# Kernel tuning notes

Hardware: AMD Instinct MI355X
Metric: run time of the kernel (lower is better)

The kernel has to match this reference:

```python
import jax, jax.numpy as jnp
import numpy as np

D_MODEL, D_K, D_V, N_HEADS = 1024, 64, 64, 16
BATCH, N_CTX = 2, 2048


def half_causal_allowed(n):
    # rows [0, n/2): attend to cols [0, n/2) only (dense block)
    # rows [n/2, n): standard causal (col <= row)
    i = jnp.arange(n)[:, None]
    j = jnp.arange(n)[None, :]
    top = (i < n // 2) & (j < n // 2)
    bot = (i >= n // 2) & (j <= i)
    return top | bot  # [n, n] bool


def setup_inputs() -> dict:
    key = jax.random.key(0)
    ks = jax.random.split(key, 8)
    s_in = 1.0 / np.sqrt(D_MODEL)
    s_out = 1.0 / np.sqrt(D_V * N_HEADS)
    return {
        "x": jax.random.normal(ks[0], (BATCH, N_CTX, D_MODEL), jnp.float32),
        # Linear weights stored [in, out] (transpose of torch layout)
        "Wq": jax.random.uniform(ks[1], (D_MODEL, D_K * N_HEADS), jnp.float32, -s_in, s_in),
        "bq": jax.random.uniform(ks[2], (D_K * N_HEADS,), jnp.float32, -s_in, s_in),
        "Wk": jax.random.uniform(ks[3], (D_MODEL, D_K * N_HEADS), jnp.float32, -s_in, s_in),
        "bk": jax.random.uniform(ks[4], (D_K * N_HEADS,), jnp.float32, -s_in, s_in),
        "Wv": jax.random.uniform(ks[5], (D_MODEL, D_V * N_HEADS), jnp.float32, -s_in, s_in),
        "bv": jax.random.uniform(ks[6], (D_V * N_HEADS,), jnp.float32, -s_in, s_in),
        "Wo": jax.random.uniform(ks[7], (D_V * N_HEADS, D_MODEL), jnp.float32, -s_out, s_out),
    }


def reference(x, Wq, bq, Wk, bk, Wv, bv, Wo):
    b, n, _ = x.shape
    h, dk, dv = N_HEADS, D_K, D_V
    # projections -> [b, h, n, d]
    q = (x @ Wq + bq).reshape(b, n, h, dk).transpose(0, 2, 1, 3)
    k = (x @ Wk + bk).reshape(b, n, h, dk).transpose(0, 2, 1, 3)
    v = (x @ Wv + bv).reshape(b, n, h, dv).transpose(0, 2, 1, 3)
    scores = jnp.einsum("bhqd,bhkd->bhqk", q / jnp.sqrt(jnp.float32(dk)), k)
    allowed = half_causal_allowed(n)  # [n, n]
    scores = jnp.where(allowed, scores, -jnp.inf)
    attn = jax.nn.softmax(scores, axis=-1)  # dropout p=0 -> identity
    out = jnp.einsum("bhqk,bhkd->bhqd", attn, v)
    out = out.transpose(0, 2, 1, 3).reshape(b, n, h * dv)
    return out @ Wo  # final Linear has no bias
```

## Files before the change

kernel.cpp:

```cpp
#include <hip/hip_runtime.h>
#include <hip/hip_bf16.h>

#define NH 16
#define DH 64
#define DM 1024
#define NC 2048
#define MROWS 4096
#define KVT 64

#define SCALE_Q 0.180336880f

typedef __attribute__((ext_vector_type(8))) short short8;
typedef __attribute__((ext_vector_type(4))) float f32x4;
typedef __attribute__((ext_vector_type(16))) float f32x16;
typedef __attribute__((ext_vector_type(4))) unsigned int uint4e;

__device__ __forceinline__ unsigned pkbf16(float a, float b) {
    unsigned r;
    asm("v_cvt_pk_bf16_f32 %0, %1, %2" : "=v"(r) : "v"(a), "v"(b));
    return r;
}
__device__ __forceinline__ unsigned short f2bf(float x) {
    return (unsigned short)(pkbf16(x, x) & 0xffffu);
}
__device__ __forceinline__ float exp2v(float x) {
    float r;
    asm("v_exp_f32 %0, %1" : "=v"(r) : "v"(x));
    return r;
}
__device__ __forceinline__ f32x16 fzero16() {
    f32x16 r;
    #pragma unroll
    for (int i = 0; i < 16; ++i) r[i] = 0.f;
    return r;
}
__device__ __forceinline__ short8 mk8(unsigned w0, unsigned w1, unsigned w2, unsigned w3) {
    uint4e u = {w0, w1, w2, w3};
    return __builtin_bit_cast(short8, u);
}
__device__ __forceinline__ void gload16(const unsigned short* g, unsigned short* l) {
    __builtin_amdgcn_global_load_lds(
        (const __attribute__((address_space(1))) void*)g,
        (__attribute__((address_space(3))) void*)l, 16, 0, 0);
}

__global__ __launch_bounds__(256) void cvt_x(const float* __restrict__ in,
                                             unsigned short* __restrict__ out, int n8)
{
    int i = blockIdx.x * 256 + threadIdx.x;
    if (i >= n8) return;
    const float4 a = ((const float4*)in)[i * 2];
    const float4 b = ((const float4*)in)[i * 2 + 1];
    uint4e u = {pkbf16(a.x, a.y), pkbf16(a.z, a.w), pkbf16(b.x, b.y), pkbf16(b.z, b.w)};
    ((uint4e*)out)[i] = u;
}

__global__ __launch_bounds__(256) void cvt_w4(const float* __restrict__ W0,
                                              const float* __restrict__ W1,
                                              const float* __restrict__ W2,
                                              const float* __restrict__ W3,
                                              unsigned short* __restrict__ Wt4)
{
    __shared__ unsigned short T[64][72];
    const int z = blockIdx.z;
    const float* W = (z == 0) ? W0 : (z == 1) ? W1 : (z == 2) ? W2 : W3;
    unsigned short* Wt = Wt4 + (size_t)z * DM * DM;
    const int t = threadIdx.x;
    const int r = t >> 2, s = t & 3;
    const int bi = blockIdx.y;
    const int bj = blockIdx.x;
    const float* src = W + (size_t)(bi * 64 + r) * DM + bj * 64 + s * 16;
    float4 f0 = ((const float4*)src)[0];
    float4 f1 = ((const float4*)src)[1];
    float4 f2 = ((const float4*)src)[2];
    float4 f3 = ((const float4*)src)[3];
    uint2 u;
    u.x = pkbf16(f0.x, f0.y); u.y = pkbf16(f0.z, f0.w); *(uint2*)&T[r][s * 16]      = u;
    u.x = pkbf16(f1.x, f1.y); u.y = pkbf16(f1.z, f1.w); *(uint2*)&T[r][s * 16 + 4]  = u;
    u.x = pkbf16(f2.x, f2.y); u.y = pkbf16(f2.z, f2.w); *(uint2*)&T[r][s * 16 + 8]  = u;
    u.x = pkbf16(f3.x, f3.y); u.y = pkbf16(f3.z, f3.w); *(uint2*)&T[r][s * 16 + 12] = u;
    __syncthreads();
    unsigned short vals[16];
    #pragma unroll
    for (int j = 0; j < 16; ++j) vals[j] = T[s * 16 + j][r];
    unsigned short* dst = Wt + (size_t)(bj * 64 + r) * DM + bi * 64 + s * 16;
    *(short8*)(dst)     = *(short8*)&vals[0];
    *(short8*)(dst + 8) = *(short8*)&vals[8];
}

__global__ __launch_bounds__(256) void gemm_qkv(const unsigned short* __restrict__ A,
                                                const unsigned short* __restrict__ Bt,
                                                const float* __restrict__ bq,
                                                const float* __restrict__ bk,
                                                const float* __restrict__ bv,
                                                unsigned short* __restrict__ Out)
{
    __shared__ unsigned short As[128 * 32];
    __shared__ unsigned short Bs[128 * 32];
    const int t  = threadIdx.x;
    const int w  = t >> 6, l = t & 63;
    const int wr = w >> 1, wc = w & 1;
    const int m0 = blockIdx.y << 7;
    const int n0 = blockIdx.x << 7;

    f32x4 acc[4][4] = {};
    const int nkt = DM >> 5;
    for (int kt = 0; kt < nkt; ++kt) {
        #pragma unroll
        for (int j = 0; j < 2; ++j) {
            const int c0 = j * 256 + w * 64;
            const int cc = c0 + l;
            const int row = cc >> 2, qq = cc & 3;
            gload16(A  + (size_t)(m0 + row) * DM + kt * 32 + qq * 8, &As[c0 * 8]);
            gload16(Bt + (size_t)(n0 + row) * DM + kt * 32 + qq * 8, &Bs[c0 * 8]);
        }
        __syncthreads();
        short8 af[4], bf_[4];
        #pragma unroll
        for (int mi = 0; mi < 4; ++mi)
            af[mi] = *(short8*)&As[(wr * 64 + mi * 16 + (l & 15)) * 32 + (l >> 4) * 8];
        #pragma unroll
        for (int ni = 0; ni < 4; ++ni)
            bf_[ni] = *(short8*)&Bs[(wc * 64 + ni * 16 + (l & 15)) * 32 + (l >> 4) * 8];
        #pragma unroll
        for (int mi = 0; mi < 4; ++mi)
            #pragma unroll
            for (int ni = 0; ni < 4; ++ni)
                acc[mi][ni] = __builtin_amdgcn_mfma_f32_16x16x32_bf16(
                                  af[mi], bf_[ni], acc[mi][ni], 0, 0, 0);
        __syncthreads();
    }

    const int seg = n0 >> 10;
    const float* bias = (seg == 0) ? bq : (seg == 1) ? bk : bv;
    const float scale = (seg == 0) ? SCALE_Q : 1.0f;
    const int ncol0 = (n0 & 1023) + wc * 64;
    float bvv[4];
    #pragma unroll
    for (int ni = 0; ni < 4; ++ni)
        bvv[ni] = bias[ncol0 + ni * 16 + (l & 15)];

    if (seg == 2) {
        unsigned short* vt = Out + 2 * (size_t)MROWS * DM;
        #pragma unroll
        for (int mi = 0; mi < 4; ++mi)
            #pragma unroll
            for (int ni = 0; ni < 4; ++ni) {
                const int gcol = ncol0 + ni * 16 + (l & 15);
                const int h_ = gcol >> 6, d_ = gcol & 63;
                #pragma unroll
                for (int r = 0; r < 4; ++r) {
                    const int grow = m0 + wr * 64 + mi * 16 + (l >> 4) * 4 + r;
                    const int b_ = grow >> 11, n_ = grow & 2047;
                    vt[(((size_t)b_ * 16 + h_) * 64 + d_) * NC + n_] =
                        f2bf(acc[mi][ni][r] + bvv[ni]);
                }
            }
    } else {
        unsigned short* C = Out + (size_t)seg * MROWS * DM;
        #pragma unroll
        for (int mi = 0; mi < 4; ++mi)
            #pragma unroll
            for (int ni = 0; ni < 4; ++ni) {
                const int gcol = ncol0 + ni * 16 + (l & 15);
                #pragma unroll
                for (int r = 0; r < 4; ++r) {
                    const int grow = m0 + wr * 64 + mi * 16 + (l >> 4) * 4 + r;
                    C[(size_t)grow * DM + gcol] = f2bf((acc[mi][ni][r] + bvv[ni]) * scale);
                }
            }
    }
}

__global__ __launch_bounds__(256) void gemm_wo(const unsigned short* __restrict__ A,
                                               const unsigned short* __restrict__ Bt,
                                               float* __restrict__ C)
{
    __shared__ unsigned short As[64 * 32];
    __shared__ unsigned short Bs[128 * 32];
    const int t = threadIdx.x, w = t >> 6, l = t & 63;
    const int wr = w >> 1, wc = w & 1;
    const int m0 = blockIdx.y << 6;
    const int n0 = blockIdx.x << 7;

    f32x4 acc[2][4] = {};
    const int nkt = DM >> 5;
    for (int kt = 0; kt < nkt; ++kt) {
        {
            const int c0 = w * 64;
            const int cc = c0 + l;
            const int row = cc >> 2, qq = cc & 3;
            gload16(A + (size_t)(m0 + row) * DM + kt * 32 + qq * 8, &As[c0 * 8]);
        }
        #pragma unroll
        for (int j = 0; j < 2; ++j) {
            const int c0 = j * 256 + w * 64;
            const int cc = c0 + l;
            const int row = cc >> 2, qq = cc & 3;
            gload16(Bt + (size_t)(n0 + row) * DM + kt * 32 + qq * 8, &Bs[c0 * 8]);
        }
        __syncthreads();
        short8 af[2], bf_[4];
        #pragma unroll
        for (int mi = 0; mi < 2; ++mi)
            af[mi] = *(short8*)&As[(wr * 32 + mi * 16 + (l & 15)) * 32 + (l >> 4) * 8];
        #pragma unroll
        for (int ni = 0; ni < 4; ++ni)
            bf_[ni] = *(short8*)&Bs[(wc * 64 + ni * 16 + (l & 15)) * 32 + (l >> 4) * 8];
        #pragma unroll
        for (int mi = 0; mi < 2; ++mi)
            #pragma unroll
            for (int ni = 0; ni < 4; ++ni)
                acc[mi][ni] = __builtin_amdgcn_mfma_f32_16x16x32_bf16(
                                  af[mi], bf_[ni], acc[mi][ni], 0, 0, 0);
        __syncthreads();
    }
    #pragma unroll
    for (int mi = 0; mi < 2; ++mi)
        #pragma unroll
        for (int ni = 0; ni < 4; ++ni) {
            const int gcol = n0 + wc * 64 + ni * 16 + (l & 15);
            #pragma unroll
            for (int r = 0; r < 4; ++r) {
                const int grow = m0 + wr * 32 + mi * 16 + (l >> 4) * 4 + r;
                C[(size_t)grow * DM + gcol] = acc[mi][ni][r];
            }
        }
}

__global__ __launch_bounds__(128, 2) void attn_nosm(const unsigned short* __restrict__ Qg,
                                                    const unsigned short* __restrict__ Kg,
                                                    const unsigned short* __restrict__ Vtg,
                                                    unsigned short* __restrict__ Og)
{
    __shared__ unsigned short KS[2][4096];
    __shared__ unsigned short VS[2][4096];
    const int t   = threadIdx.x;
    const int w   = t >> 6;
    const int l   = t & 63;
    const int l31 = l & 31;
    const int hi  = l >> 5;

    const int f   = blockIdx.x;
    const int xcd = f & 7;
    const int pos = f >> 3;
    const int bh  = xcd * 4 + (pos >> 5);
    int qt = pos & 31;
    if ((pos >> 5) & 1) qt = 31 - qt;
    const int b = bh >> 4;
    const int h = bh & 15;

    const int qb = qt << 6;
    const int wq = qb + w * 32;
    const size_t rb0 = (size_t)b * NC;
    const int hd = h * DH;

    const unsigned short* qp = Qg + (rb0 + wq + l31) * DM + hd + hi * 8;
    short8 fq[4];
    #pragma unroll
    for (int c = 0; c < 4; ++c)
        fq[c] = *(const short8*)(qp + c * 16);

    f32x16 o0 = fzero16(), o1 = fzero16();
    f32x16 lacc = fzero16();
    const bool bottom = (qb >= NC / 2);
    const int nkv = bottom ? (qt + 1) : 16;

    const unsigned short* Vbase = Vtg + (size_t)bh * 64 * NC;

    auto stage = [&](int it, int buf) {
        const int kb = it * KVT;
        #pragma unroll
        for (int j = 0; j < 4; ++j) {
            const int jj  = w * 4 + j;
            const int p   = jj * 64 + l;
            const int row = p >> 3;
            const int slot = (p & 7) ^ (row & 7);
            gload16(Kg + (size_t)(rb0 + kb + row) * DM + hd + slot * 8,
                    &KS[buf][jj * 512]);
            gload16(Vbase + (size_t)row * NC + kb + slot * 8,
                    &VS[buf][jj * 512]);
        }
    };

    stage(0, 0);
    if (nkv > 1) stage(1, 1);

    for (int it = 0; it < nkv; ++it) {
        const int kb = it * KVT;
        const int cur = it & 1;
        if (it + 1 < nkv) {
            asm volatile("s_waitcnt vmcnt(8)" ::: "memory");
        } else {
            asm volatile("s_waitcnt vmcnt(0)" ::: "memory");
        }
        __builtin_amdgcn_s_barrier();

        short8 kf[2][4], vf[2][4];
        #pragma unroll
        for (int half = 0; half < 2; ++half) {
            const int row = half * 32 + l31;
            const int rx  = row & 7;
            #pragma unroll
            for (int c = 0; c < 4; ++c) {
                const int slot = (c * 2 + hi) ^ rx;
                kf[half][c] = *(const short8*)(&KS[cur][row * 64 + slot * 8]);
                vf[half][c] = *(const short8*)(&VS[cur][row * 64 + slot * 8]);
            }
        }
        asm volatile("s_waitcnt lgkmcnt(0)" ::: "memory");
        __builtin_amdgcn_sched_barrier(0);
        __builtin_amdgcn_s_barrier();

        if (it + 2 < nkv) stage(it + 2, cur);

        const bool active = bottom ? (kb <= wq + 31) : true;
        if (active) {
            f32x16 s0 = fzero16(), s1 = fzero16();
            __builtin_amdgcn_s_setprio(1);
            #pragma unroll
            for (int c = 0; c < 4; ++c) {
                s0 = __builtin_amdgcn_mfma_f32_32x32x16_bf16(kf[0][c], fq[c], s0, 0, 0, 0);
                s1 = __builtin_amdgcn_mfma_f32_32x32x16_bf16(kf[1][c], fq[c], s1, 0, 0, 0);
            }
            __builtin_amdgcn_s_setprio(0);
            if (bottom && (kb + KVT - 1 > wq)) {
                const int qg = wq + l31;
                #pragma unroll
                for (int r = 0; r < 16; ++r) {
                    const int kk = (r & 3) + 8 * (r >> 2) + 4 * hi;
                    if (kb + kk > qg)      s0[r] = -1e30f;
                    if (kb + 32 + kk > qg) s1[r] = -1e30f;
                }
            }
            #pragma unroll
            for (int r = 0; r < 16; ++r) s0[r] = exp2v(s0[r]);
            #pragma unroll
            for (int r = 0; r < 16; ++r) s1[r] = exp2v(s1[r]);
            #pragma unroll
            for (int r = 0; r < 16; ++r) lacc[r] += s0[r] + s1[r];
            __builtin_amdgcn_s_setprio(1);
            #pragma unroll
            for (int kc = 0; kc < 4; ++kc) {
                const f32x16 src = (kc < 2) ? s0 : s1;
                const int rbase = (kc & 1) * 8;
                unsigned A01 = pkbf16(src[rbase + 0], src[rbase + 1]);
                unsigned A23 = pkbf16(src[rbase + 2], src[rbase + 3]);
                unsigned A45 = pkbf16(src[rbase + 4], src[rbase + 5]);
                unsigned A67 = pkbf16(src[rbase + 6], src[rbase + 7]);
                unsigned s01 = (unsigned)__shfl_xor((int)A01, 32);
                unsigned s23 = (unsigned)__shfl_xor((int)A23, 32);
                unsigned s45 = (unsigned)__shfl_xor((int)A45, 32);
                unsigned s67 = (unsigned)__shfl_xor((int)A67, 32);
                short8 fp = hi ? mk8(s45, s67, A45, A67)
                               : mk8(A01, A23, s01, s23);
                o0 = __builtin_amdgcn_mfma_f32_32x32x16_bf16(vf[0][kc], fp, o0, 0, 0, 0);
                o1 = __builtin_amdgcn_mfma_f32_32x32x16_bf16(vf[1][kc], fp, o1, 0, 0, 0);
            }
            __builtin_amdgcn_s_setprio(0);
        }
    }
    __syncthreads();

    float lr[8];
    #pragma unroll
    for (int r = 0; r < 8; ++r) lr[r] = lacc[r] + lacc[r + 8];
    #pragma unroll
    for (int st = 4; st > 0; st >>= 1)
        #pragma unroll
        for (int r = 0; r < 4; ++r)
            if (r < st) lr[r] += lr[r + st];
    const float lrun = lr[0] + __shfl_xor(lr[0], 32);
    const float inv = 1.f / lrun;

    unsigned short* obuf = (unsigned short*)&KS[0][0];
    {
        unsigned short* reg = obuf + (size_t)(w * 32 + l31) * 72;
        #pragma unroll
        for (int r = 0; r < 16; ++r) {
            const int dd = (r & 3) + 8 * (r >> 2) + 4 * hi;
            reg[dd]      = f2bf(o0[r] * inv);
            reg[dd + 32] = f2bf(o1[r] * inv);
        }
    }
    __syncthreads();
    {
        const int row = t >> 1, seg = t & 1;
        const unsigned short* src = obuf + (size_t)row * 72 + seg * 32;
        unsigned short* dst = Og + (rb0 + qb + row) * DM + hd + seg * 32;
        #pragma unroll
        for (int i = 0; i < 4; ++i)
            *(short8*)(dst + i * 8) = *(const short8*)(src + i * 8);
    }
}

extern "C" void kernel_launch(void* const* d_in, const int* in_sizes, int n_in,
                              void* d_out, int out_size, void* d_ws, size_t ws_size,
                              hipStream_t stream)
{
    const float* x  = (const float*)d_in[0];
    const float* Wq = (const float*)d_in[1];
    const float* bq = (const float*)d_in[2];
    const float* Wk = (const float*)d_in[3];
    const float* bk = (const float*)d_in[4];
    const float* Wv = (const float*)d_in[5];
    const float* bv = (const float*)d_in[6];
    const float* Wo = (const float*)d_in[7];
    float* out = (float*)d_out;

    char* ws = (char*)d_ws;
    const size_t szA = (size_t)MROWS * DM * 2;
    const size_t szW = (size_t)DM * DM * 2;
    unsigned short* xb  = (unsigned short*)(ws);
    unsigned short* wqT = (unsigned short*)(ws + szA);
    unsigned short* woT = (unsigned short*)(ws + szA + 3 * szW);
    unsigned short* qb_ = (unsigned short*)(ws + szA + 4 * szW);
    unsigned short* kb_ = (unsigned short*)(ws + 2 * szA + 4 * szW);
    unsigned short* vt_ = (unsigned short*)(ws + 3 * szA + 4 * szW);
    unsigned short* ab_ = (unsigned short*)(ws + 4 * szA + 4 * szW);

    cvt_x<<<dim3(MROWS * DM / 8 / 256), 256, 0, stream>>>(x, xb, MROWS * DM / 8);
    cvt_w4<<<dim3(16, 16, 4), 256, 0, stream>>>(Wq, Wk, Wv, Wo, wqT);

    gemm_qkv<<<dim3(24, 32), 256, 0, stream>>>(xb, wqT, bq, bk, bv, qb_);
    attn_nosm<<<dim3(1024), 128, 0, stream>>>(qb_, kb_, vt_, ab_);
    gemm_wo<<<dim3(8, 64), 256, 0, stream>>>(ab_, woT, out);
}
```

Measured before the change: 114.7 us.

## Split attention KV loop across two waves per 32-row query tile; fuse prep kernels

The attention kernel now gives each block a 32-row query tile and has its two waves process alternating KV tiles independently, each with its own LDS buffer and no block barriers in the loop. The partial outputs and row sums are combined through LDS at the end. This doubles the grid, cuts the per-block causal tail, and removes inter-wave synchronisation. The price is that each wave loads full K/V tiles (no shared staging), there is only single-buffer prefetch per wave, and an extra reduction step. Separately, the x and weight bf16 conversion kernels are merged into a single launch.

```diff
diff --git a/kernel.cpp b/kernel.cpp
--- a/kernel.cpp
+++ b/kernel.cpp
@@ -44,31 +44,35 @@
         (__attribute__((address_space(3))) void*)l, 16, 0, 0);
 }
 
-__global__ __launch_bounds__(256) void cvt_x(const float* __restrict__ in,
-                                             unsigned short* __restrict__ out, int n8)
-{
-    int i = blockIdx.x * 256 + threadIdx.x;
-    if (i >= n8) return;
-    const float4 a = ((const float4*)in)[i * 2];
-    const float4 b = ((const float4*)in)[i * 2 + 1];
-    uint4e u = {pkbf16(a.x, a.y), pkbf16(a.z, a.w), pkbf16(b.x, b.y), pkbf16(b.z, b.w)};
-    ((uint4e*)out)[i] = u;
-}
-
-__global__ __launch_bounds__(256) void cvt_w4(const float* __restrict__ W0,
-                                              const float* __restrict__ W1,
-                                              const float* __restrict__ W2,
-                                              const float* __restrict__ W3,
-                                              unsigned short* __restrict__ Wt4)
+__global__ __launch_bounds__(256) void prep(const float* __restrict__ x,
+                                            const float* __restrict__ W0,
+                                            const float* __restrict__ W1,
+                                            const float* __restrict__ W2,
+                                            const float* __restrict__ W3,
+                                            unsigned short* __restrict__ xb,
+                                            unsigned short* __restrict__ Wt4)
 {
     __shared__ unsigned short T[64][72];
-    const int z = blockIdx.z;
+    const int bid = blockIdx.x;
+    const int t = threadIdx.x;
+    if (bid < 1024) {
+        #pragma unroll
+        for (int g = 0; g < 2; ++g) {
+            const int i = bid * 512 + g * 256 + t;
+            const float4 a = ((const float4*)x)[i * 2];
+            const float4 b = ((const float4*)x)[i * 2 + 1];
+            uint4e u = {pkbf16(a.x, a.y), pkbf16(a.z, a.w),
+                        pkbf16(b.x, b.y), pkbf16(b.z, b.w)};
+            ((uint4e*)xb)[i] = u;
+        }
+        return;
+    }
+    const int z = (bid - 1024) >> 8;
+    const int tile = (bid - 1024) & 255;
+    const int bi = tile >> 4, bj = tile & 15;
     const float* W = (z == 0) ? W0 : (z == 1) ? W1 : (z == 2) ? W2 : W3;
     unsigned short* Wt = Wt4 + (size_t)z * DM * DM;
-    const int t = threadIdx.x;
     const int r = t >> 2, s = t & 3;
-    const int bi = blockIdx.y;
-    const int bj = blockIdx.x;
     const float* src = W + (size_t)(bi * 64 + r) * DM + bj * 64 + s * 16;
     float4 f0 = ((const float4*)src)[0];
     float4 f1 = ((const float4*)src)[1];
@@ -228,10 +232,10 @@
         }
 }
 
-__global__ __launch_bounds__(128, 2) void attn_nosm(const unsigned short* __restrict__ Qg,
-                                                    const unsigned short* __restrict__ Kg,
-                                                    const unsigned short* __restrict__ Vtg,
-                                                    unsigned short* __restrict__ Og)
+__global__ __launch_bounds__(128) void attn_split(const unsigned short* __restrict__ Qg,
+                                                  const unsigned short* __restrict__ Kg,
+                                                  const unsigned short* __restrict__ Vtg,
+                                                  unsigned short* __restrict__ Og)
 {
     __shared__ unsigned short KS[2][4096];
     __shared__ unsigned short VS[2][4096];
@@ -244,18 +248,17 @@
     const int f   = blockIdx.x;
     const int xcd = f & 7;
     const int pos = f >> 3;
-    const int bh  = xcd * 4 + (pos >> 5);
-    int qt = pos & 31;
-    if ((pos >> 5) & 1) qt = 31 - qt;
+    const int bh  = xcd * 4 + (pos >> 6);
+    int qc = pos & 63;
+    if ((pos >> 6) & 1) qc = 63 - qc;
     const int b = bh >> 4;
     const int h = bh & 15;
 
-    const int qb = qt << 6;
-    const int wq = qb + w * 32;
+    const int qb = qc << 5;
     const size_t rb0 = (size_t)b * NC;
     const int hd = h * DH;
 
-    const unsigned short* qp = Qg + (rb0 + wq + l31) * DM + hd + hi * 8;
+    const unsigned short* qp = Qg + (rb0 + qb + l31) * DM + hd + hi * 8;
     short8 fq[4];
     #pragma unroll
     for (int c = 0; c < 4; ++c)
@@ -263,38 +266,31 @@
 
     f32x16 o0 = fzero16(), o1 = fzero16();
     f32x16 lacc = fzero16();
-    const bool bottom = (qb >= NC / 2);
-    const int nkv = bottom ? (qt + 1) : 16;
+    const int nkv = (qc < 32) ? 16 : ((qc >> 1) + 1);
+    const int niter = (nkv - w + 1) >> 1;
 
     const unsigned short* Vbase = Vtg + (size_t)bh * 64 * NC;
 
-    auto stage = [&](int it, int buf) {
+    auto stage = [&](int it) {
         const int kb = it * KVT;
         #pragma unroll
-        for (int j = 0; j < 4; ++j) {
-            const int jj  = w * 4 + j;
-            const int p   = jj * 64 + l;
-            const int row = p >> 3;
+        for (int j = 0; j < 8; ++j) {
+            const int p    = j * 64 + l;
+            const int row  = p >> 3;
             const int slot = (p & 7) ^ (row & 7);
             gload16(Kg + (size_t)(rb0 + kb + row) * DM + hd + slot * 8,
-                    &KS[buf][jj * 512]);
+                    &KS[w][j * 512]);
             gload16(Vbase + (size_t)row * NC + kb + slot * 8,
-                    &VS[buf][jj * 512]);
+                    &VS[w][j * 512]);
         }
     };
 
-    stage(0, 0);
-    if (nkv > 1) stage(1, 1);
-
-    for (int it = 0; it < nkv; ++it) {
+    stage(w);
+
+    for (int i = 0; i < niter; ++i) {
+        const int it = w + 2 * i;
         const int kb = it * KVT;
-        const int cur = it & 1;
-        if (it + 1 < nkv) {
-            asm volatile("s_waitcnt vmcnt(8)" ::: "memory");
-        } else {
-            asm volatile("s_waitcnt vmcnt(0)" ::: "memory");
-        }
-        __builtin_amdgcn_s_barrier();
+        asm volatile("s_waitcnt vmcnt(0)" ::: "memory");
 
         short8 kf[2][4], vf[2][4];
         #pragma unroll
@@ -304,63 +300,57 @@
             #pragma unroll
             for (int c = 0; c < 4; ++c) {
                 const int slot = (c * 2 + hi) ^ rx;
-                kf[half][c] = *(const short8*)(&KS[cur][row * 64 + slot * 8]);
-                vf[half][c] = *(const short8*)(&VS[cur][row * 64 + slot * 8]);
+                kf[half][c] = *(const short8*)(&KS[w][row * 64 + slot * 8]);
+                vf[half][c] = *(const short8*)(&VS[w][row * 64 + slot * 8]);
             }
         }
         asm volatile("s_waitcnt lgkmcnt(0)" ::: "memory");
         __builtin_amdgcn_sched_barrier(0);
-        __builtin_amdgcn_s_barrier();
-
-        if (it + 2 < nkv) stage(it + 2, cur);
-
-        const bool active = bottom ? (kb <= wq + 31) : true;
-        if (active) {
-            f32x16 s0 = fzero16(), s1 = fzero16();
-            __builtin_amdgcn_s_setprio(1);
-            #pragma unroll
-            for (int c = 0; c < 4; ++c) {
-                s0 = __builtin_amdgcn_mfma_f32_32x32x16_bf16(kf[0][c], fq[c], s0, 0, 0, 0);
-                s1 = __builtin_amdgcn_mfma_f32_32x32x16_bf16(kf[1][c], fq[c], s1, 0, 0, 0);
+        if (i + 1 < niter) stage(w + 2 * (i + 1));
+
+        f32x16 s0 = fzero16(), s1 = fzero16();
+        __builtin_amdgcn_s_setprio(1);
+        #pragma unroll
+        for (int c = 0; c < 4; ++c) {
+            s0 = __builtin_amdgcn_mfma_f32_32x32x16_bf16(kf[0][c], fq[c], s0, 0, 0, 0);
+            s1 = __builtin_amdgcn_mfma_f32_32x32x16_bf16(kf[1][c], fq[c], s1, 0, 0, 0);
+        }
+        __builtin_amdgcn_s_setprio(0);
+        if (qc >= 32 && it == nkv - 1) {
+            const int qg = qb + l31;
+            #pragma unroll
+            for (int r = 0; r < 16; ++r) {
+                const int kk = (r & 3) + 8 * (r >> 2) + 4 * hi;
+                if (kb + kk > qg)      s0[r] = -1e30f;
+                if (kb + 32 + kk > qg) s1[r] = -1e30f;
             }
-            __builtin_amdgcn_s_setprio(0);
-            if (bottom && (kb + KVT - 1 > wq)) {
-                const int qg = wq + l31;
-                #pragma unroll
-                for (int r = 0; r < 16; ++r) {
-                    const int kk = (r & 3) + 8 * (r >> 2) + 4 * hi;
-                    if (kb + kk > qg)      s0[r] = -1e30f;
-                    if (kb + 32 + kk > qg) s1[r] = -1e30f;
-                }
-            }
-            #pragma unroll
-            for (int r = 0; r < 16; ++r) s0[r] = exp2v(s0[r]);
-            #pragma unroll
-            for (int r = 0; r < 16; ++r) s1[r] = exp2v(s1[r]);
-            #pragma unroll
-            for (int r = 0; r < 16; ++r) lacc[r] += s0[r] + s1[r];
-            __builtin_amdgcn_s_setprio(1);
-            #pragma unroll
-            for (int kc = 0; kc < 4; ++kc) {
-                const f32x16 src = (kc < 2) ? s0 : s1;
-                const int rbase = (kc & 1) * 8;
-                unsigned A01 = pkbf16(src[rbase + 0], src[rbase + 1]);
-                unsigned A23 = pkbf16(src[rbase + 2], src[rbase + 3]);
-                unsigned A45 = pkbf16(src[rbase + 4], src[rbase + 5]);
-                unsigned A67 = pkbf16(src[rbase + 6], src[rbase + 7]);
-                unsigned s01 = (unsigned)__shfl_xor((int)A01, 32);
-                unsigned s23 = (unsigned)__shfl_xor((int)A23, 32);
-                unsigned s45 = (unsigned)__shfl_xor((int)A45, 32);
-                unsigned s67 = (unsigned)__shfl_xor((int)A67, 32);
-                short8 fp = hi ? mk8(s45, s67, A45, A67)
-                               : mk8(A01, A23, s01, s23);
-                o0 = __builtin_amdgcn_mfma_f32_32x32x16_bf16(vf[0][kc], fp, o0, 0, 0, 0);
-                o1 = __builtin_amdgcn_mfma_f32_32x32x16_bf16(vf[1][kc], fp, o1, 0, 0, 0);
-            }
-            __builtin_amdgcn_s_setprio(0);
-        }
-    }
-    __syncthreads();
+        }
+        #pragma unroll
+        for (int r = 0; r < 16; ++r) s0[r] = exp2v(s0[r]);
+        #pragma unroll
+        for (int r = 0; r < 16; ++r) s1[r] = exp2v(s1[r]);
+        #pragma unroll
+        for (int r = 0; r < 16; ++r) lacc[r] += s0[r] + s1[r];
+        __builtin_amdgcn_s_setprio(1);
+        #pragma unroll
+        for (int kc = 0; kc < 4; ++kc) {
+            const f32x16 src = (kc < 2) ? s0 : s1;
+            const int rbase = (kc & 1) * 8;
+            unsigned A01 = pkbf16(src[rbase + 0], src[rbase + 1]);
+            unsigned A23 = pkbf16(src[rbase + 2], src[rbase + 3]);
+            unsigned A45 = pkbf16(src[rbase + 4], src[rbase + 5]);
+            unsigned A67 = pkbf16(src[rbase + 6], src[rbase + 7]);
+            unsigned s01 = (unsigned)__shfl_xor((int)A01, 32);
+            unsigned s23 = (unsigned)__shfl_xor((int)A23, 32);
+            unsigned s45 = (unsigned)__shfl_xor((int)A45, 32);
+            unsigned s67 = (unsigned)__shfl_xor((int)A67, 32);
+            short8 fp = hi ? mk8(s45, s67, A45, A67)
+                           : mk8(A01, A23, s01, s23);
+            o0 = __builtin_amdgcn_mfma_f32_32x32x16_bf16(vf[0][kc], fp, o0, 0, 0, 0);
+            o1 = __builtin_amdgcn_mfma_f32_32x32x16_bf16(vf[1][kc], fp, o1, 0, 0, 0);
+        }
+        __builtin_amdgcn_s_setprio(0);
+    }
 
     float lr[8];
     #pragma unroll
@@ -370,22 +360,38 @@
         #pragma unroll
         for (int r = 0; r < 4; ++r)
             if (r < st) lr[r] += lr[r + st];
-    const float lrun = lr[0] + __shfl_xor(lr[0], 32);
-    const float inv = 1.f / lrun;
-
-    unsigned short* obuf = (unsigned short*)&KS[0][0];
+    const float lpart = lr[0] + __shfl_xor(lr[0], 32);
+
     {
-        unsigned short* reg = obuf + (size_t)(w * 32 + l31) * 72;
+        float* po = (float*)&KS[w][0];
+        #pragma unroll
+        for (int r = 0; r < 16; ++r) {
+            po[l * 32 + r]      = o0[r];
+            po[l * 32 + 16 + r] = o1[r];
+        }
+        ((float*)&VS[w][0])[l] = lpart;
+    }
+    __syncthreads();
+
+    if (w == 0) {
+        const float* po1 = (const float*)&KS[1][0];
+        float oc0[16], oc1[16];
+        #pragma unroll
+        for (int r = 0; r < 16; ++r) {
+            oc0[r] = o0[r] + po1[l * 32 + r];
+            oc1[r] = o1[r] + po1[l * 32 + 16 + r];
+        }
+        const float lt = lpart + ((const float*)&VS[1][0])[l];
+        const float inv = 1.f / lt;
+        unsigned short* obuf = &VS[0][0];
+        unsigned short* reg = obuf + (size_t)l31 * 72;
         #pragma unroll
         for (int r = 0; r < 16; ++r) {
             const int dd = (r & 3) + 8 * (r >> 2) + 4 * hi;
-            reg[dd]      = f2bf(o0[r] * inv);
-            reg[dd + 32] = f2bf(o1[r] * inv);
-        }
-    }
-    __syncthreads();
-    {
-        const int row = t >> 1, seg = t & 1;
+            reg[dd]      = f2bf(oc0[r] * inv);
+            reg[dd + 32] = f2bf(oc1[r] * inv);
+        }
+        const int row = l >> 1, seg = l & 1;
         const unsigned short* src = obuf + (size_t)row * 72 + seg * 32;
         unsigned short* dst = Og + (rb0 + qb + row) * DM + hd + seg * 32;
         #pragma unroll
@@ -419,10 +425,8 @@
     unsigned short* vt_ = (unsigned short*)(ws + 3 * szA + 4 * szW);
     unsigned short* ab_ = (unsigned short*)(ws + 4 * szA + 4 * szW);
 
-    cvt_x<<<dim3(MROWS * DM / 8 / 256), 256, 0, stream>>>(x, xb, MROWS * DM / 8);
-    cvt_w4<<<dim3(16, 16, 4), 256, 0, stream>>>(Wq, Wk, Wv, Wo, wqT);
-
+    prep<<<dim3(2048), 256, 0, stream>>>(x, Wq, Wk, Wv, Wo, xb, wqT);
     gemm_qkv<<<dim3(24, 32), 256, 0, stream>>>(xb, wqT, bq, bk, bv, qb_);
-    attn_nosm<<<dim3(1024), 128, 0, stream>>>(qb_, kb_, vt_, ab_);
+    attn_split<<<dim3(2048), 128, 0, stream>>>(qb_, kb_, vt_, ab_);
     gemm_wo<<<dim3(8, 64), 256, 0, stream>>>(ab_, woT, out);
 }
```

Result: slower. 118.9 us (+3.7%).

## Double GEMM K-tile to 64 with XOR-swizzled LDS and merge prep kernels

Applied to the files above, without the earlier changes.

Both GEMMs now stage 64-wide K tiles instead of 32, which halves the loop iterations and the barriers per tile. The LDS layout uses an XOR swizzle on 16-byte slots to avoid bank conflicts on the fragment reads. The x conversion and the weight-transpose kernels are merged into one launch to save a kernel launch. The trade-off is twice the LDS per block, which may lower occupancy, plus more fragment registers.

```diff
diff --git a/kernel.cpp b/kernel.cpp
--- a/kernel.cpp
+++ b/kernel.cpp
@@ -44,31 +44,35 @@
         (__attribute__((address_space(3))) void*)l, 16, 0, 0);
 }
 
-__global__ __launch_bounds__(256) void cvt_x(const float* __restrict__ in,
-                                             unsigned short* __restrict__ out, int n8)
-{
-    int i = blockIdx.x * 256 + threadIdx.x;
-    if (i >= n8) return;
-    const float4 a = ((const float4*)in)[i * 2];
-    const float4 b = ((const float4*)in)[i * 2 + 1];
-    uint4e u = {pkbf16(a.x, a.y), pkbf16(a.z, a.w), pkbf16(b.x, b.y), pkbf16(b.z, b.w)};
-    ((uint4e*)out)[i] = u;
-}
-
-__global__ __launch_bounds__(256) void cvt_w4(const float* __restrict__ W0,
-                                              const float* __restrict__ W1,
-                                              const float* __restrict__ W2,
-                                              const float* __restrict__ W3,
-                                              unsigned short* __restrict__ Wt4)
+__global__ __launch_bounds__(256) void prep(const float* __restrict__ x,
+                                            const float* __restrict__ W0,
+                                            const float* __restrict__ W1,
+                                            const float* __restrict__ W2,
+                                            const float* __restrict__ W3,
+                                            unsigned short* __restrict__ xb,
+                                            unsigned short* __restrict__ Wt4)
 {
     __shared__ unsigned short T[64][72];
-    const int z = blockIdx.z;
+    const int bid = blockIdx.x;
+    const int t = threadIdx.x;
+    if (bid < 1024) {
+        #pragma unroll
+        for (int g = 0; g < 2; ++g) {
+            const int i = bid * 512 + g * 256 + t;
+            const float4 a = ((const float4*)x)[i * 2];
+            const float4 b = ((const float4*)x)[i * 2 + 1];
+            uint4e u = {pkbf16(a.x, a.y), pkbf16(a.z, a.w),
+                        pkbf16(b.x, b.y), pkbf16(b.z, b.w)};
+            ((uint4e*)xb)[i] = u;
+        }
+        return;
+    }
+    const int z = (bid - 1024) >> 8;
+    const int tile = (bid - 1024) & 255;
+    const int bi = tile >> 4, bj = tile & 15;
     const float* W = (z == 0) ? W0 : (z == 1) ? W1 : (z == 2) ? W2 : W3;
     unsigned short* Wt = Wt4 + (size_t)z * DM * DM;
-    const int t = threadIdx.x;
     const int r = t >> 2, s = t & 3;
-    const int bi = blockIdx.y;
-    const int bj = blockIdx.x;
     const float* src = W + (size_t)(bi * 64 + r) * DM + bj * 64 + s * 16;
     float4 f0 = ((const float4*)src)[0];
     float4 f1 = ((const float4*)src)[1];
@@ -95,8 +99,8 @@
                                                 const float* __restrict__ bv,
                                                 unsigned short* __restrict__ Out)
 {
-    __shared__ unsigned short As[128 * 32];
-    __shared__ unsigned short Bs[128 * 32];
+    __shared__ unsigned short As[128 * 64];
+    __shared__ unsigned short Bs[128 * 64];
     const int t  = threadIdx.x;
     const int w  = t >> 6, l = t & 63;
     const int wr = w >> 1, wc = w & 1;
@@ -104,30 +108,43 @@
     const int n0 = blockIdx.x << 7;
 
     f32x4 acc[4][4] = {};
-    const int nkt = DM >> 5;
+    const int nkt = DM >> 6;
     for (int kt = 0; kt < nkt; ++kt) {
         #pragma unroll
-        for (int j = 0; j < 2; ++j) {
+        for (int j = 0; j < 4; ++j) {
             const int c0 = j * 256 + w * 64;
-            const int cc = c0 + l;
-            const int row = cc >> 2, qq = cc & 3;
-            gload16(A  + (size_t)(m0 + row) * DM + kt * 32 + qq * 8, &As[c0 * 8]);
-            gload16(Bt + (size_t)(n0 + row) * DM + kt * 32 + qq * 8, &Bs[c0 * 8]);
+            const int p  = c0 + l;
+            const int row = p >> 3;
+            const int slot = (p & 7) ^ (row & 7);
+            gload16(A  + (size_t)(m0 + row) * DM + kt * 64 + slot * 8, &As[c0 * 8]);
+            gload16(Bt + (size_t)(n0 + row) * DM + kt * 64 + slot * 8, &Bs[c0 * 8]);
         }
         __syncthreads();
-        short8 af[4], bf_[4];
-        #pragma unroll
-        for (int mi = 0; mi < 4; ++mi)
-            af[mi] = *(short8*)&As[(wr * 64 + mi * 16 + (l & 15)) * 32 + (l >> 4) * 8];
-        #pragma unroll
-        for (int ni = 0; ni < 4; ++ni)
-            bf_[ni] = *(short8*)&Bs[(wc * 64 + ni * 16 + (l & 15)) * 32 + (l >> 4) * 8];
-        #pragma unroll
-        for (int mi = 0; mi < 4; ++mi)
-            #pragma unroll
-            for (int ni = 0; ni < 4; ++ni)
-                acc[mi][ni] = __builtin_amdgcn_mfma_f32_16x16x32_bf16(
-                                  af[mi], bf_[ni], acc[mi][ni], 0, 0, 0);
+        short8 af[4][2], bf_[4][2];
+        #pragma unroll
+        for (int mi = 0; mi < 4; ++mi) {
+            const int row = wr * 64 + mi * 16 + (l & 15);
+            const int rx  = row & 7;
+            #pragma unroll
+            for (int k2 = 0; k2 < 2; ++k2)
+                af[mi][k2] = *(short8*)&As[row * 64 + ((k2 * 4 + (l >> 4)) ^ rx) * 8];
+        }
+        #pragma unroll
+        for (int ni = 0; ni < 4; ++ni) {
+            const int row = wc * 64 + ni * 16 + (l & 15);
+            const int rx  = row & 7;
+            #pragma unroll
+            for (int k2 = 0; k2 < 2; ++k2)
+                bf_[ni][k2] = *(short8*)&Bs[row * 64 + ((k2 * 4 + (l >> 4)) ^ rx) * 8];
+        }
+        #pragma unroll
+        for (int k2 = 0; k2 < 2; ++k2)
+            #pragma unroll
+            for (int mi = 0; mi < 4; ++mi)
+                #pragma unroll
+                for (int ni = 0; ni < 4; ++ni)
+                    acc[mi][ni] = __builtin_amdgcn_mfma_f32_16x16x32_bf16(
+                                      af[mi][k2], bf_[ni][k2], acc[mi][ni], 0, 0, 0);
         __syncthreads();
     }
 
@@ -176,43 +193,58 @@
                                                const unsigned short* __restrict__ Bt,
                                                float* __restrict__ C)
 {
-    __shared__ unsigned short As[64 * 32];
-    __shared__ unsigned short Bs[128 * 32];
+    __shared__ unsigned short As[64 * 64];
+    __shared__ unsigned short Bs[128 * 64];
     const int t = threadIdx.x, w = t >> 6, l = t & 63;
     const int wr = w >> 1, wc = w & 1;
     const int m0 = blockIdx.y << 6;
     const int n0 = blockIdx.x << 7;
 
     f32x4 acc[2][4] = {};
-    const int nkt = DM >> 5;
+    const int nkt = DM >> 6;
     for (int kt = 0; kt < nkt; ++kt) {
-        {
-            const int c0 = w * 64;
-            const int cc = c0 + l;
-            const int row = cc >> 2, qq = cc & 3;
-            gload16(A + (size_t)(m0 + row) * DM + kt * 32 + qq * 8, &As[c0 * 8]);
-        }
         #pragma unroll
         for (int j = 0; j < 2; ++j) {
             const int c0 = j * 256 + w * 64;
-            const int cc = c0 + l;
-            const int row = cc >> 2, qq = cc & 3;
-            gload16(Bt + (size_t)(n0 + row) * DM + kt * 32 + qq * 8, &Bs[c0 * 8]);
+            const int p  = c0 + l;
+            const int row = p >> 3;
+            const int slot = (p & 7) ^ (row & 7);
+            gload16(A + (size_t)(m0 + row) * DM + kt * 64 + slot * 8, &As[c0 * 8]);
+        }
+        #pragma unroll
+        for (int j = 0; j < 4; ++j) {
+            const int c0 = j * 256 + w * 64;
+            const int p  = c0 + l;
+            const int row = p >> 3;
+            const int slot = (p & 7) ^ (row & 7);
+            gload16(Bt + (size_t)(n0 + row) * DM + kt * 64 + slot * 8, &Bs[c0 * 8]);
         }
         __syncthreads();
-        short8 af[2], bf_[4];
-        #pragma unroll
-        for (int mi = 0; mi < 2; ++mi)
-            af[mi] = *(short8*)&As[(wr * 32 + mi * 16 + (l & 15)) * 32 + (l >> 4) * 8];
-        #pragma unroll
-        for (int ni = 0; ni < 4; ++ni)
-            bf_[ni] = *(short8*)&Bs[(wc * 64 + ni * 16 + (l & 15)) * 32 + (l >> 4) * 8];
-        #pragma unroll
-        for (int mi = 0; mi < 2; ++mi)
-            #pragma unroll
-            for (int ni = 0; ni < 4; ++ni)
-                acc[mi][ni] = __builtin_amdgcn_mfma_f32_16x16x32_bf16(
-                                  af[mi], bf_[ni], acc[mi][ni], 0, 0, 0);
+        short8 af[2][2], bf_[4][2];
+        #pragma unroll
+        for (int mi = 0; mi < 2; ++mi) {
+            const int row = wr * 32 + mi * 16 + (l & 15);
+            const int rx  = row & 7;
+            #pragma unroll
+            for (int k2 = 0; k2 < 2; ++k2)
+                af[mi][k2] = *(short8*)&As[row * 64 + ((k2 * 4 + (l >> 4)) ^ rx) * 8];
+        }
+        #pragma unroll
+        for (int ni = 0; ni < 4; ++ni) {
+            const int row = wc * 64 + ni * 16 + (l & 15);
+            const int rx  = row & 7;
+            #pragma unroll
+            for (int k2 = 0; k2 < 2; ++k2)
+                bf_[ni][k2] = *(short8*)&Bs[row * 64 + ((k2 * 4 + (l >> 4)) ^ rx) * 8];
+        }
+        #pragma unroll
+        for (int k2 = 0; k2 < 2; ++k2)
+            #pragma unroll
+            for (int mi = 0; mi < 2; ++mi)
+                #pragma unroll
+                for (int ni = 0; ni < 4; ++ni)
+                    acc[mi][ni] = __builtin_amdgcn_mfma_f32_16x16x32_bf16(
+                                      af[mi][k2], bf_[ni][k2], acc[mi][ni], 0, 0, 0);
         __syncthreads();
     }
     #pragma unroll
@@ -419,9 +451,7 @@
     unsigned short* vt_ = (unsigned short*)(ws + 3 * szA + 4 * szW);
     unsigned short* ab_ = (unsigned short*)(ws + 4 * szA + 4 * szW);
 
-    cvt_x<<<dim3(MROWS * DM / 8 / 256), 256, 0, stream>>>(x, xb, MROWS * DM / 8);
-    cvt_w4<<<dim3(16, 16, 4), 256, 0, stream>>>(Wq, Wk, Wv, Wo, wqT);
-
+    prep<<<dim3(2048), 256, 0, stream>>>(x, Wq, Wk, Wv, Wo, xb, wqT);
     gemm_qkv<<<dim3(24, 32), 256, 0, stream>>>(xb, wqT, bq, bk, bv, qb_);
     attn_nosm<<<dim3(1024), 128, 0, stream>>>(qb_, kb_, vt_, ab_);
     gemm_wo<<<dim3(8, 64), 256, 0, stream>>>(ab_, woT, out);
```

Measured after the change: 120.3 us. 4.9% more time.
